# Performance work log

Measured on AMD Instinct MI355X. Metric: run time of the kernel, lower is better.

Reference implementation:

```python
import jax, jax.numpy as jnp
import numpy as np
import math

N_HEADS = 16
D_HEAD = 64
D_MODEL = 1024
ROPE_THETA = 10000.0


def setup_inputs() -> dict:
    key = jax.random.key(0)
    k1, k2, k3 = jax.random.split(key, 3)
    B, T = 2, 2048
    x = jax.random.normal(k1, (B, T, D_MODEL), dtype=jnp.float32)
    # torch Linear(in, out) weight has shape (out, in); store transposed (in, out)
    # so forward is x @ w. Scale like default init to keep activations sane.
    w_qkv = jax.random.normal(k2, (D_MODEL, 3 * D_MODEL), dtype=jnp.float32) / math.sqrt(D_MODEL)
    w_o = jax.random.normal(k3, (D_MODEL, D_MODEL), dtype=jnp.float32) / math.sqrt(D_MODEL)
    return {"x": x, "w_qkv": w_qkv, "w_o": w_o}


def _build_rope(T, dtype):
    inv_freq = 1.0 / (ROPE_THETA ** (jnp.arange(0, D_HEAD, 2, dtype=jnp.float32) / D_HEAD))
    t = jnp.arange(T, dtype=jnp.float32)
    freqs = jnp.outer(t, inv_freq)            # [T, D_HEAD/2]
    emb = jnp.concatenate([freqs, freqs], -1)  # [T, D_HEAD]
    return jnp.cos(emb).astype(dtype), jnp.sin(emb).astype(dtype)


def _apply_rope(x, cos, sin):
    # x: [B, T, H, D_HEAD]; cos/sin broadcast as [1, T, 1, D_HEAD]
    x1, x2 = jnp.split(x, 2, axis=-1)
    rotated = jnp.concatenate([-x2, x1], axis=-1)
    return x * cos + rotated * sin


def reference(x, w_qkv, w_o):
    B, T, D = x.shape
    qkv = (x @ w_qkv).reshape(B, T, 3, N_HEADS, D_HEAD)
    q, k, v = qkv[:, :, 0], qkv[:, :, 1], qkv[:, :, 2]  # [B, T, H, Dh]
    cos, sin = _build_rope(T, x.dtype)
    cos = cos[None, :, None, :]
    sin = sin[None, :, None, :]
    q = _apply_rope(q, cos, sin)
    k = _apply_rope(k, cos, sin)
    scale = 1.0 / math.sqrt(D_HEAD)
    # full [B, H, T, T] scores (faithful to the manual matmul-softmax-matmul)
    attn = jnp.einsum("bthd,bshd->bhts", q, k) * scale
    attn = jax.nn.softmax(attn, axis=-1)
    out = jnp.einsum("bhts,bshd->bthd", attn, v).reshape(B, T, D)
    return out @ w_o
```

## Files before the change

### kernel.cpp

```cpp
#include <hip/hip_runtime.h>
#include <cstdint>

typedef unsigned short ushort_t;
typedef __attribute__((ext_vector_type(8))) short v8s;
typedef __attribute__((ext_vector_type(4))) short v4s;
typedef __attribute__((ext_vector_type(2))) unsigned v2u;
typedef __attribute__((ext_vector_type(4))) float v4f;

#define MFMA(a, b, c) __builtin_amdgcn_mfma_f32_16x16x32_bf16(a, b, c, 0, 0, 0)
#define QSCALE 0.18033688011112042f

#define GLL(gp, lp) __builtin_amdgcn_global_load_lds(                        \
    (const __attribute__((address_space(1))) void*)(gp),                     \
    (__attribute__((address_space(3))) void*)(lp), 16, 0, 0)

#define WAIT_LGKM0() __builtin_amdgcn_s_waitcnt(0xc07f)

__device__ __forceinline__ float bf2f(ushort_t u) {
    union { unsigned u; float f; } x; x.u = ((unsigned)u) << 16; return x.f;
}
__device__ __forceinline__ short f2bf(float f) {
    union { float f; unsigned u; } x; x.f = f;
    unsigned r = x.u + 0x7fffu + ((x.u >> 16) & 1u);
    return (short)(r >> 16);
}

__global__ __launch_bounds__(256) void prep(const void* __restrict__ xin,
                                            const void* __restrict__ w1,
                                            const void* __restrict__ w2,
                                            ushort_t* __restrict__ xb,
                                            ushort_t* __restrict__ out1,
                                            ushort_t* __restrict__ out2,
                                            int* __restrict__ flag,
                                            float* __restrict__ tab) {
    __shared__ ushort_t tile[64][65];
    __shared__ int cnt;
    int bid = blockIdx.x, tid = threadIdx.x;

    int isbf = 0;
    if (bid < 3072 || bid == 3328) {
        if (tid == 0) cnt = 0;
        __syncthreads();
        unsigned w = ((const unsigned*)xin)[tid];
        int e = (w >> 7) & 0xFF;
        int hit = ((e >= 96 && e <= 135) || (w & 0xFFFFu) == 0) ? 1 : 0;
        atomicAdd(&cnt, hit);
        __syncthreads();
        isbf = (cnt >= 160) ? 1 : 0;
        if (bid == 3328) {
            if (tid == 0) *flag = isbf;
            return;
        }
    }

    if (bid < 2048) {
        int i = bid * 256 + tid;
        if (isbf) {
            ((v8s*)xb)[i] = ((const v8s*)xin)[i];
        } else {
            const float* xf = (const float*)xin + (size_t)i * 8;
            v8s o;
            #pragma unroll
            for (int j = 0; j < 8; ++j) o[j] = f2bf(xf[j]);
            ((v8s*)xb)[i] = o;
        }
    } else if (bid < 3072) {
        int t = bid - 2048;
        int bxl = t & 63, by = (t >> 6) * 64;
        const void* in; ushort_t* out; int C, bx;
        if (bxl < 48) { in = w1; out = out1; C = 3072; bx = bxl * 64; }
        else          { in = w2; out = out2; C = 1024; bx = (bxl - 48) * 64; }
        const int R = 1024;
        int tx = tid & 63, ty = tid >> 6;
        for (int i = ty; i < 64; i += 4) {
            size_t idx = (size_t)(by + i) * C + bx + tx;
            tile[i][tx] = isbf ? ((const ushort_t*)in)[idx]
                               : (ushort_t)f2bf(((const float*)in)[idx]);
        }
        __syncthreads();
        for (int i = ty; i < 64; i += 4) out[(size_t)(bx + i) * R + by + tx] = tile[tx][i];
    } else {
        int idx = (bid - 3072) * 256 + tid;
        int d = idx >> 11, t = idx & 2047;
        float inv_freq = __expf(-(float)d * 0.28782313662425575f);
        float ang = (float)t * inv_freq;
        float sn, cs;
        sincosf(ang, &sn, &cs);
        tab[d * 2048 + t]         = bf2f((ushort_t)f2bf(cs));
        tab[65536 + d * 2048 + t] = bf2f((ushort_t)f2bf(sn));
    }
}

template <int MODE, int BN>
__global__ __launch_bounds__(256) void gemm_bt(const ushort_t* __restrict__ A,
                                               const ushort_t* __restrict__ BT,
                                               void* __restrict__ C,
                                               const int* __restrict__ flagp,
                                               int M, int N, int K,
                                               ushort_t* __restrict__ Qp,
                                               ushort_t* __restrict__ Kp,
                                               ushort_t* __restrict__ Vp,
                                               const float* __restrict__ tab) {
    constexpr int NJ = BN / 32;
    __shared__ __align__(16) ushort_t As[2][128 * 32];
    __shared__ __align__(16) ushort_t Bs[2][BN * 32];
    int tid = threadIdx.x;
    int lane = tid & 63;
    int lr = lane & 15, lc = lane >> 4;
    int w = tid >> 6;
    int wr = (w >> 1) * 64, wc = (w & 1) * (BN / 2);

    int nx = gridDim.x;
    int orig = blockIdx.y * nx + blockIdx.x;
    int cpx = (nx * gridDim.y) >> 3;
    int swz = (orig & 7) * cpx + (orig >> 3);
    int m0 = (swz / nx) * 128, n0 = (swz % nx) * BN;

    int c0 = tid, c1 = tid + 256;
    int r0 = c0 >> 2, s0 = c0 & 3;
    int r1 = c1 >> 2, s1 = c1 & 3;

    const ushort_t* Ag0 = A + (size_t)(m0 + r0) * K + s0 * 8;
    const ushort_t* Ag1 = A + (size_t)(m0 + r1) * K + s1 * 8;
    const ushort_t* Bg0 = BT + (size_t)(n0 + r0) * K + s0 * 8;
    const ushort_t* Bg1 = BT + (size_t)(n0 + r1) * K + s1 * 8;
    const int aoff0 = w * 512;
    const int aoff1 = 2048 + w * 512;
    const int boff0 = w * 512;
    const int boff1 = 2048 + w * 512;

    v4f acc[4][NJ] = {};

    GLL(Ag0, &As[0][aoff0]);
    GLL(Ag1, &As[0][aoff1]);
    GLL(Bg0, &Bs[0][boff0]);
    if constexpr (BN == 128) GLL(Bg1, &Bs[0][boff1]);
    __syncthreads();

    int buf = 0;
    for (int kt = 0; kt < K; kt += 32) {
        if (kt + 32 < K) {
            int nb = buf ^ 1;
            GLL(Ag0 + kt + 32, &As[nb][aoff0]);
            GLL(Ag1 + kt + 32, &As[nb][aoff1]);
            GLL(Bg0 + kt + 32, &Bs[nb][boff0]);
            if constexpr (BN == 128) GLL(Bg1 + kt + 32, &Bs[nb][boff1]);
        }

        v8s af[4], bfr[NJ];
        #pragma unroll
        for (int i = 0; i < 4; ++i)
            af[i] = *(const v8s*)(&As[buf][0] + (wr + i * 16 + lr) * 32 + lc * 8);
        #pragma unroll
        for (int j = 0; j < NJ; ++j)
            bfr[j] = *(const v8s*)(&Bs[buf][0] + (wc + j * 16 + lr) * 32 + lc * 8);
        #pragma unroll
        for (int i = 0; i < 4; ++i)
            #pragma unroll
            for (int j = 0; j < NJ; ++j)
                acc[i][j] = MFMA(af[i], bfr[j], acc[i][j]);

        __syncthreads();
        buf ^= 1;
    }

    if (MODE == 1) {
        int store_f32 = (*flagp == 0);
        #pragma unroll
        for (int i = 0; i < 4; ++i)
            #pragma unroll
            for (int j = 0; j < NJ; ++j)
                #pragma unroll
                for (int r = 0; r < 4; ++r) {
                    int row = m0 + wr + i * 16 + lc * 4 + r;
                    int col = n0 + wc + j * 16 + lr;
                    if (store_f32)
                        ((float*)C)[(size_t)row * N + col] = acc[i][j][r];
                    else
                        ((ushort_t*)C)[(size_t)row * N + col] = (ushort_t)f2bf(acc[i][j][r]);
                }
    } else {
        int region = n0 >> 10;
        int h = ((n0 & 1023) + wc) >> 6;
        if (region < 2) {
            const float sc = (region == 0) ? QSCALE : 1.0f;
            ushort_t* dst = (region == 0) ? Qp : Kp;
            #pragma unroll
            for (int i = 0; i < 4; ++i)
                #pragma unroll
                for (int j = 0; j < 2; ++j) {
                    int d = j * 16 + lr;
                    int tg0 = m0 + wr + i * 16 + lc * 4;
                    int b = tg0 >> 11, tt0 = tg0 & 2047;
                    v4f cs4 = *(const v4f*)(tab + d * 2048 + tt0);
                    v4f sn4 = *(const v4f*)(tab + 65536 + d * 2048 + tt0);
                    #pragma unroll
                    for (int r = 0; r < 4; ++r) {
                        float x1 = acc[i][j][r], x2 = acc[i][(j + 2) % NJ][r];
                        size_t base = ((size_t)(b * 16 + h) * 2048 + tt0 + r) * 64 + d;
                        dst[base]      = (ushort_t)f2bf((x1 * cs4[r] - x2 * sn4[r]) * sc);
                        dst[base + 32] = (ushort_t)f2bf((x2 * cs4[r] + x1 * sn4[r]) * sc);
                    }
                }
        } else {
            #pragma unroll
            for (int i = 0; i < 4; ++i)
                #pragma unroll
                for (int j = 0; j < NJ; ++j) {
                    int d = j * 16 + lr;
                    int tg0 = m0 + wr + i * 16 + lc * 4;
                    int b = tg0 >> 11, tt = tg0 & 2047;
                    v4s pk;
                    #pragma unroll
                    for (int r = 0; r < 4; ++r) pk[r] = f2bf(acc[i][j][r]);
                    size_t base = (size_t)(b * 16 + h) * 131072 + (size_t)(tt >> 5) * 2048
                                + (size_t)d * 32 + (tt & 31);
                    *(v4s*)(Vp + base) = pk;
                }
        }
    }
}

__global__ __launch_bounds__(256) void gemm_o(const ushort_t* __restrict__ A,
                                              const ushort_t* __restrict__ BT,
                                              void* __restrict__ C,
                                              const int* __restrict__ flagp) {
    constexpr int K = 1024, N = 1024;
    __shared__ __align__(16) ushort_t As[2][128 * 64];
    __shared__ __align__(16) ushort_t Bs[2][64 * 64];
    int tid = threadIdx.x;
    int lane = tid & 63;
    int lr = lane & 15, lc = lane >> 4;
    int w = tid >> 6;
    int wr = (w >> 1) * 64, wc = (w & 1) * 32;

    int nx = gridDim.x;
    int orig = blockIdx.y * nx + blockIdx.x;
    int cpx = (nx * gridDim.y) >> 3;
    int swz = (orig & 7) * cpx + (orig >> 3);
    int m0 = (swz / nx) * 128, n0 = (swz % nx) * 64;

    const ushort_t* ag[4]; const ushort_t* bg[2];
    int al[4], bl[2];
    #pragma unroll
    for (int q = 0; q < 4; ++q) {
        int c = q * 256 + tid, r = c >> 3, p = c & 7;
        ag[q] = A + (size_t)(m0 + r) * K + ((p ^ (r & 7)) * 8);
        al[q] = (q * 256 + w * 64) * 8;
    }
    #pragma unroll
    for (int q = 0; q < 2; ++q) {
        int c = q * 256 + tid, r = c >> 3, p = c & 7;
        bg[q] = BT + (size_t)(n0 + r) * K + ((p ^ (r & 7)) * 8);
        bl[q] = (q * 256 + w * 64) * 8;
    }

    v4f acc[4][2] = {};

    #pragma unroll
    for (int q = 0; q < 4; ++q) GLL(ag[q], &As[0][al[q]]);
    #pragma unroll
    for (int q = 0; q < 2; ++q) GLL(bg[q], &Bs[0][bl[q]]);
    __syncthreads();

    int buf = 0;
    for (int t = 0; t < 16; ++t) {
        if (t + 1 < 16) {
            int kg = (t + 1) * 64, nb = buf ^ 1;
            #pragma unroll
            for (int q = 0; q < 4; ++q) GLL(ag[q] + kg, &As[nb][al[q]]);
            #pragma unroll
            for (int q = 0; q < 2; ++q) GLL(bg[q] + kg, &Bs[nb][bl[q]]);
        }

        v8s af[4][2], bf[2][2];
        #pragma unroll
        for (int i = 0; i < 4; ++i)
            #pragma unroll
            for (int kk = 0; kk < 2; ++kk)
                af[i][kk] = *(const v8s*)(&As[buf][0] + (wr + i * 16 + lr) * 64
                                          + (((kk * 4 + lc) ^ (lr & 7)) * 8));
        #pragma unroll
        for (int j = 0; j < 2; ++j)
            #pragma unroll
            for (int kk = 0; kk < 2; ++kk)
                bf[j][kk] = *(const v8s*)(&Bs[buf][0] + (wc + j * 16 + lr) * 64
                                          + (((kk * 4 + lc) ^ (lr & 7)) * 8));
        __builtin_amdgcn_s_setprio(1);
        #pragma unroll
        for (int i = 0; i < 4; ++i)
            #pragma unroll
            for (int j = 0; j < 2; ++j) {
                acc[i][j] = MFMA(af[i][0], bf[j][0], acc[i][j]);
                acc[i][j] = MFMA(af[i][1], bf[j][1], acc[i][j]);
            }
        __builtin_amdgcn_s_setprio(0);

        __syncthreads();
        buf ^= 1;
    }

    int store_f32 = (*flagp == 0);
    #pragma unroll
    for (int i = 0; i < 4; ++i)
        #pragma unroll
        for (int j = 0; j < 2; ++j)
            #pragma unroll
            for (int r = 0; r < 4; ++r) {
                int row = m0 + wr + i * 16 + lc * 4 + r;
                int col = n0 + wc + j * 16 + lr;
                if (store_f32)
                    ((float*)C)[(size_t)row * N + col] = acc[i][j][r];
                else
                    ((ushort_t*)C)[(size_t)row * N + col] = (ushort_t)f2bf(acc[i][j][r]);
            }
}

__global__ __launch_bounds__(256) void attn(const ushort_t* __restrict__ Qr,
                                            const ushort_t* __restrict__ Kr,
                                            const ushort_t* __restrict__ Vt,
                                            ushort_t* __restrict__ AO) {
    __shared__ __align__(16) char lds[36864];
    int tid = threadIdx.x, lane = tid & 63, W = tid >> 6;
    int lr = lane & 15, lc = lane >> 4;
    int qsub = W & 1, sh = W >> 1;
    int L = blockIdx.x;
    int bh = (L & 7) * 4 + ((L >> 3) & 3);
    int qt = L >> 5;
    int q0 = qt * 128 + qsub * 64;
    int b = bh >> 4, h = bh & 15;
    const ushort_t* Qb = Qr + ((size_t)bh * 2048 + q0) * 64;
    const ushort_t* Kb = Kr + (size_t)bh * 131072 + (size_t)sh * 65536;
    const ushort_t* Vb = Vt + (size_t)bh * 131072 + (size_t)sh * 65536;
    ushort_t* KsG = (ushort_t*)(lds + sh * 16384);
    ushort_t* VsG = (ushort_t*)(lds + sh * 16384 + 8192);

    int gt = tid & 127;
    int c0 = gt, c1 = gt + 128;
    int kr0 = c0 >> 3, kc0 = c0 & 7, kr1 = c1 >> 3, kc1 = c1 & 7;
    const ushort_t* Kg0 = Kb + (size_t)kr0 * 64 + kc0 * 8;
    const ushort_t* Kg1 = Kb + (size_t)kr1 * 64 + kc1 * 8;
    int kl0 = kr0 * 64 + (kc0 ^ (kr0 & 7)) * 8;
    int kl1 = kr1 * 64 + (kc1 ^ (kr1 & 7)) * 8;
    const ushort_t* Vg0 = Vb + (size_t)c0 * 8;
    const ushort_t* Vg1 = Vb + (size_t)c1 * 8;
    int vl0 = c0 * 8, vl1 = c1 * 8;

    int blr = (lr >> 2) * 8 + (lr & 3);

    v8s qf[4][2];
    #pragma unroll
    for (int jq = 0; jq < 4; ++jq)
        #pragma unroll
        for (int kk = 0; kk < 2; ++kk)
            qf[jq][kk] = *(const v8s*)(Qb + (size_t)(jq * 16 + lr) * 64 + kk * 32 + lc * 8);

    v4f o[4][4] = {};
    float li[4] = {0.f, 0.f, 0.f, 0.f};

    v8s ka = *(const v8s*)(Kg0), kb2 = *(const v8s*)(Kg1);
    v8s va = *(const v8s*)(Vg0), vb2 = *(const v8s*)(Vg1);
    *(v8s*)(KsG + kl0) = ka;
    *(v8s*)(KsG + kl1) = kb2;
    *(v8s*)(VsG + vl0) = va;
    *(v8s*)(VsG + vl1) = vb2;
    ka  = *(const v8s*)(Kg0 + 2048);
    kb2 = *(const v8s*)(Kg1 + 2048);
    va  = *(const v8s*)(Vg0 + 2048);
    vb2 = *(const v8s*)(Vg1 + 2048);
    __syncthreads();

    #pragma unroll 1
    for (int t = 0; t < 32; ++t) {
        int p = t & 1;
        const ushort_t* Kl = KsG + p * 2048;
        const ushort_t* Vl = VsG + p * 2048;

        v8s kf[2][2], vf[4];
        #pragma unroll
        for (int hh = 0; hh < 2; ++hh) {
            int rn = blr + hh * 4;
            int sw = hh * 4 + (lr & 3);
            #pragma unroll
            for (int kk = 0; kk < 2; ++kk)
                kf[hh][kk] = *(const v8s*)(Kl + rn * 64 + (((kk * 4 + lc) ^ sw) * 8));
        }
        #pragma unroll
        for (int i = 0; i < 4; ++i)
            vf[i] = *(const v8s*)(Vl + (i * 16 + lr) * 32 + lc * 8);

        v4f St[2][4] = {};
        __builtin_amdgcn_s_setprio(1);
        #pragma unroll
        for (int hh = 0; hh < 2; ++hh)
            #pragma unroll
            for (int jq = 0; jq < 4; ++jq) {
                St[hh][jq] = MFMA(kf[hh][0], qf[jq][0], St[hh][jq]);
                St[hh][jq] = MFMA(kf[hh][1], qf[jq][1], St[hh][jq]);
            }
        __builtin_amdgcn_s_setprio(0);

        if (t + 1 < 32) {
            ushort_t* Kn = KsG + (p ^ 1) * 2048;
            ushort_t* Vn = VsG + (p ^ 1) * 2048;
            *(v8s*)(Kn + kl0) = ka;
            *(v8s*)(Kn + kl1) = kb2;
            *(v8s*)(Vn + vl0) = va;
            *(v8s*)(Vn + vl1) = vb2;
        }
        if (t + 2 < 32) {
            ka  = *(const v8s*)(Kg0 + (size_t)(t + 2) * 2048);
            kb2 = *(const v8s*)(Kg1 + (size_t)(t + 2) * 2048);
            va  = *(const v8s*)(Vg0 + (size_t)(t + 2) * 2048);
            vb2 = *(const v8s*)(Vg1 + (size_t)(t + 2) * 2048);
        }

        v8s pf[4];
        #pragma unroll
        for (int jq = 0; jq < 4; ++jq) {
            union { unsigned u[4]; v8s v; } P;
            #pragma unroll
            for (int hh = 0; hh < 2; ++hh) {
                #pragma unroll
                for (int r = 0; r < 4; ++r) {
                    float ev = __builtin_amdgcn_exp2f(St[hh][jq][r]);
                    St[hh][jq][r] = ev;
                    li[jq] += ev;
                }
                P.u[hh * 2 + 0] = __builtin_amdgcn_perm(__float_as_uint(St[hh][jq][1]),
                                                        __float_as_uint(St[hh][jq][0]), 0x07060302u);
                P.u[hh * 2 + 1] = __builtin_amdgcn_perm(__float_as_uint(St[hh][jq][3]),
                                                        __float_as_uint(St[hh][jq][2]), 0x07060302u);
            }
            pf[jq] = P.v;
        }
        __builtin_amdgcn_s_setprio(1);
        #pragma unroll
        for (int jq = 0; jq < 4; ++jq)
            #pragma unroll
            for (int i = 0; i < 4; ++i)
                o[i][jq] = MFMA(vf[i], pf[jq], o[i][jq]);
        __builtin_amdgcn_s_setprio(0);
        WAIT_LGKM0();
        __builtin_amdgcn_s_barrier();
    }

    #pragma unroll
    for (int jq = 0; jq < 4; ++jq) {
        li[jq] += __shfl_xor(li[jq], 16);
        li[jq] += __shfl_xor(li[jq], 32);
    }
    float* MO = (float*)(lds + qsub * 17408);
    float* Ml = (float*)(lds + 34816 + qsub * 256);
    __syncthreads();
    if (sh == 1) {
        #pragma unroll
        for (int jq = 0; jq < 4; ++jq) {
            #pragma unroll
            for (int i = 0; i < 4; ++i)
                *(v4f*)(MO + (jq * 16 + lr) * 68 + i * 16 + lc * 4) = o[i][jq];
            if (lc == 0) Ml[jq * 16 + lr] = li[jq];
        }
    }
    __syncthreads();
    if (sh == 0) {
        #pragma unroll
        for (int jq = 0; jq < 4; ++jq) {
            float inv = 1.0f / (li[jq] + Ml[jq * 16 + lr]);
            int t = q0 + jq * 16 + lr;
            #pragma unroll
            for (int i = 0; i < 4; ++i) {
                v4f m = *(const v4f*)(MO + (jq * 16 + lr) * 68 + i * 16 + lc * 4);
                v4s pk;
                #pragma unroll
                for (int r = 0; r < 4; ++r) pk[r] = f2bf((o[i][jq][r] + m[r]) * inv);
                *(v4s*)(AO + (size_t)(b * 2048 + t) * 1024 + h * 64 + i * 16 + lc * 4) = pk;
            }
        }
    }
}

extern "C" void kernel_launch(void* const* d_in, const int* in_sizes, int n_in,
                              void* d_out, int out_size, void* d_ws, size_t ws_size,
                              hipStream_t stream) {
    char* ws = (char*)d_ws;
    int*      flag  = (int*)ws;
    ushort_t* wqkvT = (ushort_t*)(ws + 256);
    ushort_t* woT   = (ushort_t*)(ws + 6291712);
    ushort_t* xb    = (ushort_t*)(ws + 8388864);
    ushort_t* Qr    = (ushort_t*)(ws + 16777472);
    ushort_t* Kr    = (ushort_t*)(ws + 25166080);
    ushort_t* Vt    = (ushort_t*)(ws + 33554688);
    ushort_t* AO    = (ushort_t*)(ws + 41943296);
    float*    tab   = (float*)(ws + 50331904);

    prep<<<3329, 256, 0, stream>>>(d_in[0], d_in[1], d_in[2], xb, wqkvT, woT, flag, tab);
    gemm_bt<2, 128><<<dim3(24, 32), 256, 0, stream>>>(xb, wqkvT, nullptr, flag, 4096, 3072, 1024,
                                                      Qr, Kr, Vt, tab);
    attn<<<512, 256, 0, stream>>>(Qr, Kr, Vt, AO);
    gemm_o<<<dim3(16, 32), 256, 0, stream>>>(AO, woT, d_out, flag);
}
```

Before: 189.9 us.

## Split attention KV range across four wave pairs with 512-thread blocks

The attention kernel now launches 512 threads per block, so four KV shards are each processed by a pair of waves over 16 tiles instead of two shards over 32 tiles. The cross-shard merge becomes a two-phase LDS reduction that sums three partial outputs and row sums into the shard-0 waves. This shortens the serial KV loop per wave and adds parallelism per block. In exchange it uses 64KB of LDS and larger blocks, which lowers block occupancy, and it adds a bigger reduction epilogue with extra barriers.

```diff
diff --git a/kernel.cpp b/kernel.cpp
--- a/kernel.cpp
+++ b/kernel.cpp
@@ -316,11 +316,11 @@
             }
 }
 
-__global__ __launch_bounds__(256) void attn(const ushort_t* __restrict__ Qr,
+__global__ __launch_bounds__(512) void attn(const ushort_t* __restrict__ Qr,
                                             const ushort_t* __restrict__ Kr,
                                             const ushort_t* __restrict__ Vt,
                                             ushort_t* __restrict__ AO) {
-    __shared__ __align__(16) char lds[36864];
+    __shared__ __align__(16) char lds[65536];
     int tid = threadIdx.x, lane = tid & 63, W = tid >> 6;
     int lr = lane & 15, lc = lane >> 4;
     int qsub = W & 1, sh = W >> 1;
@@ -330,8 +330,8 @@
     int q0 = qt * 128 + qsub * 64;
     int b = bh >> 4, h = bh & 15;
     const ushort_t* Qb = Qr + ((size_t)bh * 2048 + q0) * 64;
-    const ushort_t* Kb = Kr + (size_t)bh * 131072 + (size_t)sh * 65536;
-    const ushort_t* Vb = Vt + (size_t)bh * 131072 + (size_t)sh * 65536;
+    const ushort_t* Kb = Kr + (size_t)bh * 131072 + (size_t)sh * 32768;
+    const ushort_t* Vb = Vt + (size_t)bh * 131072 + (size_t)sh * 32768;
     ushort_t* KsG = (ushort_t*)(lds + sh * 16384);
     ushort_t* VsG = (ushort_t*)(lds + sh * 16384 + 8192);
 
@@ -371,7 +371,7 @@
     __syncthreads();
 
     #pragma unroll 1
-    for (int t = 0; t < 32; ++t) {
+    for (int t = 0; t < 16; ++t) {
         int p = t & 1;
         const ushort_t* Kl = KsG + p * 2048;
         const ushort_t* Vl = VsG + p * 2048;
@@ -400,7 +400,7 @@
             }
         __builtin_amdgcn_s_setprio(0);
 
-        if (t + 1 < 32) {
+        if (t + 1 < 16) {
             ushort_t* Kn = KsG + (p ^ 1) * 2048;
             ushort_t* Vn = VsG + (p ^ 1) * 2048;
             *(v8s*)(Kn + kl0) = ka;
@@ -408,7 +408,7 @@
             *(v8s*)(Vn + vl0) = va;
             *(v8s*)(Vn + vl1) = vb2;
         }
-        if (t + 2 < 32) {
+        if (t + 2 < 16) {
             ka  = *(const v8s*)(Kg0 + (size_t)(t + 2) * 2048);
             kb2 = *(const v8s*)(Kg1 + (size_t)(t + 2) * 2048);
             va  = *(const v8s*)(Vg0 + (size_t)(t + 2) * 2048);
@@ -450,33 +450,44 @@
         li[jq] += __shfl_xor(li[jq], 16);
         li[jq] += __shfl_xor(li[jq], 32);
     }
-    float* MO = (float*)(lds + qsub * 17408);
-    float* Ml = (float*)(lds + 34816 + qsub * 256);
+
+    float* MO = (float*)lds;
+    float* Ml = (float*)(lds + 52224);
     __syncthreads();
-    if (sh == 1) {
-        #pragma unroll
-        for (int jq = 0; jq < 4; ++jq) {
-            #pragma unroll
-            for (int i = 0; i < 4; ++i)
-                *(v4f*)(MO + (jq * 16 + lr) * 68 + i * 16 + lc * 4) = o[i][jq];
-            if (lc == 0) Ml[jq * 16 + lr] = li[jq];
-        }
-    }
-    __syncthreads();
-    if (sh == 0) {
-        #pragma unroll
-        for (int jq = 0; jq < 4; ++jq) {
-            float inv = 1.0f / (li[jq] + Ml[jq * 16 + lr]);
-            int t = q0 + jq * 16 + lr;
-            #pragma unroll
-            for (int i = 0; i < 4; ++i) {
-                v4f m = *(const v4f*)(MO + (jq * 16 + lr) * 68 + i * 16 + lc * 4);
-                v4s pk;
+    #pragma unroll 1
+    for (int ph = 0; ph < 2; ++ph) {
+        if (qsub == ph && sh != 0) {
+            float* M = MO + (sh - 1) * 4352;
+            #pragma unroll
+            for (int jq = 0; jq < 4; ++jq) {
                 #pragma unroll
-                for (int r = 0; r < 4; ++r) pk[r] = f2bf((o[i][jq][r] + m[r]) * inv);
-                *(v4s*)(AO + (size_t)(b * 2048 + t) * 1024 + h * 64 + i * 16 + lc * 4) = pk;
+                for (int i = 0; i < 4; ++i)
+                    *(v4f*)(M + (jq * 16 + lr) * 68 + i * 16 + lc * 4) = o[i][jq];
+                if (lc == 0) Ml[(sh - 1) * 64 + jq * 16 + lr] = li[jq];
             }
         }
+        __syncthreads();
+        if (qsub == ph && sh == 0) {
+            #pragma unroll
+            for (int jq = 0; jq < 4; ++jq) {
+                int row = jq * 16 + lr;
+                float ls = li[jq] + Ml[row] + Ml[64 + row] + Ml[128 + row];
+                float inv = 1.0f / ls;
+                int tq = q0 + row;
+                #pragma unroll
+                for (int i = 0; i < 4; ++i) {
+                    v4f m0v = *(const v4f*)(MO + row * 68 + i * 16 + lc * 4);
+                    v4f m1v = *(const v4f*)(MO + 4352 + row * 68 + i * 16 + lc * 4);
+                    v4f m2v = *(const v4f*)(MO + 8704 + row * 68 + i * 16 + lc * 4);
+                    v4s pk;
+                    #pragma unroll
+                    for (int r = 0; r < 4; ++r)
+                        pk[r] = f2bf((o[i][jq][r] + m0v[r] + m1v[r] + m2v[r]) * inv);
+                    *(v4s*)(AO + (size_t)(b * 2048 + tq) * 1024 + h * 64 + i * 16 + lc * 4) = pk;
+                }
+            }
+        }
+        __syncthreads();
     }
 }
 
@@ -497,6 +508,6 @@
     prep<<<3329, 256, 0, stream>>>(d_in[0], d_in[1], d_in[2], xb, wqkvT, woT, flag, tab);
     gemm_bt<2, 128><<<dim3(24, 32), 256, 0, stream>>>(xb, wqkvT, nullptr, flag, 4096, 3072, 1024,
                                                       Qr, Kr, Vt, tab);
-    attn<<<512, 256, 0, stream>>>(Qr, Kr, Vt, AO);
+    attn<<<512, 512, 0, stream>>>(Qr, Kr, Vt, AO);
     gemm_o<<<dim3(16, 32), 256, 0, stream>>>(AO, woT, d_out, flag);
 }
```

New measurement: 187.2 us. Within noise of the previous version (-1.4%).
